# Kernel optimization log

Hardware: AMD Instinct MI355X
Metric: run time of the kernel (lower is better)

Reference implementation:

```python
import jax, jax.numpy as jnp
import numpy as np

B, T_IN, F, NB = 32768, 3, 6, 10
H = 256
BD = H // 2            # baseline_dim
T_OUT = 5
DIN = F + H + BD       # decoder LSTMCell input size
EPS = 1e-5


def _lstm_cell(x, h, c, W_ih, W_hh, b_ih, b_hh):
    # PyTorch gate order: i, f, g, o
    z = x @ W_ih.T + h @ W_hh.T + b_ih + b_hh
    i, f, g, o = jnp.split(z, 4, axis=-1)
    c = jax.nn.sigmoid(f) * c + jax.nn.sigmoid(i) * jnp.tanh(g)
    h = jax.nn.sigmoid(o) * jnp.tanh(c)
    return h, c


def _lstm_layer(xs, W_ih, W_hh, b_ih, b_hh):
    # xs: (T, B, D_in) -> outputs (T, B, H), final (h, c)
    Bn = xs.shape[1]
    h0 = jnp.zeros((Bn, H), xs.dtype)
    c0 = jnp.zeros((Bn, H), xs.dtype)

    def step(carry, x):
        h, c = carry
        h, c = _lstm_cell(x, h, c, W_ih, W_hh, b_ih, b_hh)
        return (h, c), h

    (hT, cT), ys = jax.lax.scan(step, (h0, c0), xs)
    return ys, hT, cT


def setup_inputs() -> dict:
    key = jax.random.key(0)
    ks = jax.random.split(key, 16)
    s = 0.05
    d = {
        "cbc_input": jax.random.normal(ks[0], (B, T_IN, F), jnp.float32),
        "baseline": jax.random.normal(ks[1], (B, NB), jnp.float32),
        # encoder LSTM layer 0 / 1
        "W_ih0": jax.random.normal(ks[2], (4 * H, F), jnp.float32) * s,
        "W_hh0": jax.random.normal(ks[3], (4 * H, H), jnp.float32) * s,
        "b_ih0": jnp.zeros((4 * H,), jnp.float32),
        "b_hh0": jnp.zeros((4 * H,), jnp.float32),
        "W_ih1": jax.random.normal(ks[4], (4 * H, H), jnp.float32) * s,
        "W_hh1": jax.random.normal(ks[5], (4 * H, H), jnp.float32) * s,
        "b_ih1": jnp.zeros((4 * H,), jnp.float32),
        "b_hh1": jnp.zeros((4 * H,), jnp.float32),
        # baseline encoder: Linear + ReLU + LayerNorm
        "Wb": jax.random.normal(ks[6], (BD, NB), jnp.float32) * s,
        "bb": jnp.zeros((BD,), jnp.float32),
        "ln_g": jnp.ones((BD,), jnp.float32),
        "ln_b": jnp.zeros((BD,), jnp.float32),
        # Bahdanau attention
        "W1a": jax.random.normal(ks[7], (H, H), jnp.float32) * s,
        "b1a": jnp.zeros((H,), jnp.float32),
        "W2a": jax.random.normal(ks[8], (H, H), jnp.float32) * s,
        "b2a": jnp.zeros((H,), jnp.float32),
        "va": jax.random.normal(ks[9], (1, H), jnp.float32) * s,
        "ba": jnp.zeros((1,), jnp.float32),
        # decoder LSTMCell
        "Wd_ih": jax.random.normal(ks[10], (4 * H, DIN), jnp.float32) * s,
        "Wd_hh": jax.random.normal(ks[11], (4 * H, H), jnp.float32) * s,
        "bd_ih": jnp.zeros((4 * H,), jnp.float32),
        "bd_hh": jnp.zeros((4 * H,), jnp.float32),
        # output projection MLP
        "Wo1": jax.random.normal(ks[12], (BD, H), jnp.float32) * s,
        "bo1": jnp.zeros((BD,), jnp.float32),
        "Wo2": jax.random.normal(ks[13], (F, BD), jnp.float32) * s,
        "bo2": jnp.zeros((F,), jnp.float32),
    }
    return d


def reference(cbc_input, baseline, W_ih0, W_hh0, b_ih0, b_hh0,
              W_ih1, W_hh1, b_ih1, b_hh1, Wb, bb, ln_g, ln_b,
              W1a, b1a, W2a, b2a, va, ba,
              Wd_ih, Wd_hh, bd_ih, bd_hh, Wo1, bo1, Wo2, bo2):
    # ---- encoder (2-layer LSTM, batch_first; eval mode so no dropout) ----
    xs = jnp.swapaxes(cbc_input, 0, 1)                      # (T, B, F)
    y0, _, _ = _lstm_layer(xs, W_ih0, W_hh0, b_ih0, b_hh0)  # (T, B, H)
    y1, hT, cT = _lstm_layer(y0, W_ih1, W_hh1, b_ih1, b_hh1)
    encoder_outputs = jnp.swapaxes(y1, 0, 1)                # (B, T, H)

    # ---- baseline encoder: Linear -> ReLU -> LayerNorm ----
    z = jax.nn.relu(baseline @ Wb.T + bb)
    mu = jnp.mean(z, axis=-1, keepdims=True)
    var = jnp.mean((z - mu) ** 2, axis=-1, keepdims=True)
    baseline_repr = (z - mu) * jax.lax.rsqrt(var + EPS) * ln_g + ln_b  # (B, BD)

    enc_proj = encoder_outputs @ W2a.T + b2a                # (B, T, H) precomputed
    last_cbc0 = cbc_input[:, -1, :]                         # (B, F)

    def step(carry, _):
        h, c, last_cbc = carry
        # Bahdanau attention
        q = (h @ W1a.T + b1a)[:, None, :]                   # (B, 1, H)
        scores = jnp.tanh(q + enc_proj) @ va.T + ba         # (B, T, 1)
        weights = jax.nn.softmax(scores, axis=1)
        context = jnp.sum(weights * encoder_outputs, axis=1)  # (B, H)
        dec_in = jnp.concatenate([last_cbc, context, baseline_repr], axis=1)
        h, c = _lstm_cell(dec_in, h, c, Wd_ih, Wd_hh, bd_ih, bd_hh)
        delta = jax.nn.relu(h @ Wo1.T + bo1) @ Wo2.T + bo2
        pred = last_cbc + delta
        return (h, c, pred), pred

    _, preds = jax.lax.scan(step, (hT, cT, last_cbc0), None, length=T_OUT)
    return jnp.swapaxes(preds, 0, 1)                        # (B, 5, F)
```

## Files before the change

### kernel.cpp

```cpp
#include <hip/hip_runtime.h>

typedef unsigned short u16;
typedef __bf16 bf16x8 __attribute__((ext_vector_type(8)));
typedef float f32x4 __attribute__((ext_vector_type(4)));

#define BATCH 32768L

__device__ __forceinline__ u16 f2b(float f) {
  union { float f; unsigned int u; } v; v.f = f;
  unsigned int r = v.u + 0x7fffu + ((v.u >> 16) & 1u);
  return (u16)(r >> 16);
}
__device__ __forceinline__ float b2f(u16 h) {
  union { unsigned int u; float f; } v; v.u = ((unsigned int)h) << 16;
  return v.f;
}
__device__ __forceinline__ float sigf(float x) { return 1.f / (1.f + __expf(-x)); }
__device__ __forceinline__ float tanh_f(float x) { return 2.f / (1.f + __expf(-2.f * x)) - 1.f; }

__device__ __forceinline__ void gload16(const void* g, void* l) {
  __builtin_amdgcn_global_load_lds((const __attribute__((address_space(1))) unsigned int*)g,
                                   (__attribute__((address_space(3))) unsigned int*)l,
                                   16, 0, 0);
}

struct PrepP {
  const float* s[9]; u16* d[9]; int sc[9]; int dc[9]; long n[9];
  const float* ba[3]; const float* bb_[3]; float* bo[3];
};

__global__ void prep_kernel(PrepP p, long cvtTotal, long total) {
  for (long i = (long)blockIdx.x * blockDim.x + threadIdx.x; i < total;
       i += (long)gridDim.x * blockDim.x) {
    if (i < cvtTotal) {
      long off = i; int sg = 0;
      while (off >= p.n[sg]) { off -= p.n[sg]; ++sg; }
      long r = off / p.dc[sg]; int c = (int)(off - r * p.dc[sg]);
      p.d[sg][off] = (c < p.sc[sg]) ? f2b(p.s[sg][r * (long)p.sc[sg] + c]) : (u16)0;
    } else {
      long j = i - cvtTotal; int sg = (int)(j >> 10); int k = (int)(j & 1023);
      p.bo[sg][k] = p.ba[sg][k] + p.bb_[sg][k];
    }
  }
}

template <int EPI, int NG>
__global__ __launch_bounds__(256, 2)
void mfma_gemm4(const u16* __restrict__ A1, long lda1, int K1,
                const u16* __restrict__ W1, int wld1,
                const u16* __restrict__ A2, long lda2, int K2,
                const u16* __restrict__ W2, int wld2,
                int gs, int ys, const float* __restrict__ bias,
                u16* __restrict__ out0, int ldo, int relu,
                const float* __restrict__ cprev, float* __restrict__ cout,
                u16* __restrict__ hout, int ldh)
{
  __shared__ u16 As[3][128 * 32];
  __shared__ u16 Bs[3][NG * 64 * 32];
  const int tid = threadIdx.x;
  const int l = tid & 63, w = tid >> 6;
  const long bm = (long)blockIdx.x * 128;
  const int yb = blockIdx.y;

  const int nch1 = K1 >> 5;
  const int nch2 = A2 ? (K2 >> 5) : 0;
  const int nt = nch1 + nch2;

  f32x4 acc[8][NG];
#pragma unroll
  for (int rf = 0; rf < 8; ++rf)
#pragma unroll
    for (int g = 0; g < NG; ++g) acc[rf][g] = (f32x4){0.f, 0.f, 0.f, 0.f};

  const int l4q = l >> 2;
  const int swzs = ((l & 3) ^ ((l >> 2) & 3)) * 16;

  const char* pA[2];
  const char* pB[NG];
  auto initA = [&](const u16* A, long lda) {
#pragma unroll
    for (int c = 0; c < 2; ++c)
      pA[c] = (const char*)A + ((bm + w * 32 + c * 16 + l4q) * lda) * 2 + swzs;
  };
  auto initB = [&](const u16* W, int wld) {
#pragma unroll
    for (int c = 0; c < NG; ++c) {
      const int brow = w * (NG * 16) + c * 16 + l4q;
      const long wrow = (long)(brow >> 6) * gs + (long)yb * ys + (brow & 63);
      pB[c] = (const char*)W + (wrow * (long)wld) * 2 + swzs;
    }
  };
  auto stage = [&](int buf) {
#pragma unroll
    for (int c = 0; c < 2; ++c) {
      gload16(pA[c], &As[buf][(w * 32 + c * 16) * 32]);
      pA[c] += 64;
    }
#pragma unroll
    for (int c = 0; c < NG; ++c) {
      gload16(pB[c], &Bs[buf][(w * (NG * 16) + c * 16) * 32]);
      pB[c] += 64;
    }
  };

  initA(A1, lda1);
  initB(W1, wld1);
  stage(0);
  if (A2 && nch1 == 1) { initA(A2, lda2); initB(W2, wld2); }
  if (nt > 1) stage(1);

  const int rb = l & 15;
  const int koff = ((l >> 4) ^ (l & 3)) * 8;
  int bufR = 0, bufS = 2;
  for (int ch = 0; ch < nt; ++ch) {
    if (ch + 1 < nt) {
      asm volatile("s_waitcnt vmcnt(%0)\n\ts_barrier" :: "i"(2 + NG) : "memory");
    } else {
      asm volatile("s_waitcnt vmcnt(0)\n\ts_barrier" ::: "memory");
    }
    const int s = ch + 2;
    if (s < nt) {
      if (A2 && s == nch1) { initA(A2, lda2); initB(W2, wld2); }
      stage(bufS);
    }
    const u16* Ab = As[bufR];
    const u16* Bb = Bs[bufR];
    bf16x8 af[8];
#pragma unroll
    for (int rf = 0; rf < 8; ++rf)
      af[rf] = *(const bf16x8*)&Ab[(rf * 16 + rb) * 32 + koff];
#pragma unroll
    for (int g = 0; g < NG; ++g) {
      bf16x8 bfr = *(const bf16x8*)&Bb[(g * 64 + w * 16 + rb) * 32 + koff];
#pragma unroll
      for (int rf = 0; rf < 8; ++rf)
        acc[rf][g] = __builtin_amdgcn_mfma_f32_16x16x32_bf16(af[rf], bfr, acc[rf][g], 0, 0, 0);
    }
    bufR = (bufR == 2) ? 0 : bufR + 1;
    bufS = (bufS == 2) ? 0 : bufS + 1;
  }

  const int colb = l & 15;
  const int rq = l >> 4;
  if constexpr (EPI == 0) {
#pragma unroll
    for (int g = 0; g < NG; ++g) {
      const int wrow = g * gs + yb * ys + w * 16 + colb;
      const float bi = bias[wrow];
#pragma unroll
      for (int rf = 0; rf < 8; ++rf) {
#pragma unroll
        for (int r = 0; r < 4; ++r) {
          const long row = bm + rf * 16 + rq * 4 + r;
          float vv = acc[rf][g][r] + bi;
          if (relu) vv = fmaxf(vv, 0.f);
          out0[row * (long)ldo + wrow] = f2b(vv);
        }
      }
    }
  } else {
    const int cb = yb * 64 + w * 16 + colb;
    const float b_i = bias[cb];
    const float b_f = bias[256 + cb];
    const float b_g = bias[512 + cb];
    const float b_o = bias[768 + cb];
#pragma unroll
    for (int rf = 0; rf < 8; ++rf) {
#pragma unroll
      for (int r = 0; r < 4; ++r) {
        const long row = bm + rf * 16 + rq * 4 + r;
        const float zi = acc[rf][0][r] + b_i;
        const float zf = acc[rf][1][r] + b_f;
        const float zg = acc[rf][2][r] + b_g;
        const float zo = acc[rf][3][r] + b_o;
        const float cp = cprev ? cprev[row * 256 + cb] : 0.f;
        const float cn = sigf(zf) * cp + sigf(zi) * tanh_f(zg);
        const float hn = sigf(zo) * tanh_f(cn);
        cout[row * 256 + cb] = cn;
        hout[row * (long)ldh + cb] = f2b(hn);
      }
    }
  }
}

__global__ __launch_bounds__(256)
void front_kernel(const float* __restrict__ cbc, const float* __restrict__ baseline,
                  const float* __restrict__ Wb, const float* __restrict__ bb,
                  const float* __restrict__ ln_g, const float* __restrict__ ln_b,
                  u16* __restrict__ dec_in, u16* __restrict__ xbf)
{
  __shared__ float wbs[1280];
  __shared__ float bbs[128], lgs[128], lbs[128];
  const int tid = threadIdx.x;
  for (int i = tid; i < 1280; i += 256) wbs[i] = Wb[i];
  if (tid < 128) { bbs[tid] = bb[tid]; lgs[tid] = ln_g[tid]; lbs[tid] = ln_b[tid]; }
  __syncthreads();
  const int l = tid & 63, w = tid >> 6;
  const long row = (long)blockIdx.x * 4 + w;
#pragma unroll
  for (int e = l; e < 96; e += 64) {
    const int t = e >> 5, c = e & 31;
    xbf[(row * 3 + t) * 32 + c] = (c < 6) ? f2b(cbc[row * 18 + t * 6 + c]) : (u16)0;
  }
  if (l < 6) dec_in[row * 416 + l] = f2b(cbc[row * 18 + 12 + l]);
  else if (l < 32) dec_in[row * 416 + 390 + (l - 6)] = 0;
  float bl[10];
#pragma unroll
  for (int k = 0; k < 10; ++k) bl[k] = baseline[row * 10 + k];
  const int c0 = l, c1 = l + 64;
  float z0 = bbs[c0], z1 = bbs[c1];
#pragma unroll
  for (int k = 0; k < 10; ++k) { z0 += bl[k] * wbs[c0 * 10 + k]; z1 += bl[k] * wbs[c1 * 10 + k]; }
  z0 = fmaxf(z0, 0.f); z1 = fmaxf(z1, 0.f);
  float s = z0 + z1, sq = z0 * z0 + z1 * z1;
#pragma unroll
  for (int m = 32; m; m >>= 1) { s += __shfl_xor(s, m); sq += __shfl_xor(sq, m); }
  const float mu = s * (1.f / 128.f);
  const float var = sq * (1.f / 128.f) - mu * mu;
  const float rs = rsqrtf(var + 1e-5f);
  dec_in[row * 416 + 262 + c0] = f2b((z0 - mu) * rs * lgs[c0] + lbs[c0]);
  dec_in[row * 416 + 262 + c1] = f2b((z1 - mu) * rs * lgs[c1] + lbs[c1]);
}

__global__ __launch_bounds__(256)
void attn_kernel(const u16* __restrict__ q, const u16* __restrict__ ep,
                 const u16* __restrict__ eo, const float* __restrict__ va,
                 const float* __restrict__ ba, u16* __restrict__ dec_in)
{
  const int tid = threadIdx.x;
  const int l = tid & 63, w = tid >> 6;
  const long row = (long)blockIdx.x * 4 + w;
  const int c = l * 4;
  float qv[4], vav[4];
  {
    ushort4 qu = *(const ushort4*)&q[row * 256 + c];
    qv[0] = b2f(qu.x); qv[1] = b2f(qu.y); qv[2] = b2f(qu.z); qv[3] = b2f(qu.w);
    float4 vv = *(const float4*)&va[c];
    vav[0] = vv.x; vav[1] = vv.y; vav[2] = vv.z; vav[3] = vv.w;
  }
  float s[3];
#pragma unroll
  for (int t = 0; t < 3; ++t) {
    ushort4 eu = *(const ushort4*)&ep[row * 768 + t * 256 + c];
    float p = tanh_f(qv[0] + b2f(eu.x)) * vav[0]
            + tanh_f(qv[1] + b2f(eu.y)) * vav[1]
            + tanh_f(qv[2] + b2f(eu.z)) * vav[2]
            + tanh_f(qv[3] + b2f(eu.w)) * vav[3];
#pragma unroll
    for (int m = 32; m; m >>= 1) p += __shfl_xor(p, m);
    s[t] = p + ba[0];
  }
  const float mx = fmaxf(s[0], fmaxf(s[1], s[2]));
  const float e0 = __expf(s[0] - mx), e1 = __expf(s[1] - mx), e2 = __expf(s[2] - mx);
  const float inv = 1.f / (e0 + e1 + e2);
  const float w0 = e0 * inv, w1 = e1 * inv, w2 = e2 * inv;
  const ushort4 a0 = *(const ushort4*)&eo[row * 768 + 0 * 256 + c];
  const ushort4 a1 = *(const ushort4*)&eo[row * 768 + 1 * 256 + c];
  const ushort4 a2 = *(const ushort4*)&eo[row * 768 + 2 * 256 + c];
  u16* dp = &dec_in[row * 416 + 6 + c];
  dp[0] = f2b(w0 * b2f(a0.x) + w1 * b2f(a1.x) + w2 * b2f(a2.x));
  dp[1] = f2b(w0 * b2f(a0.y) + w1 * b2f(a1.y) + w2 * b2f(a2.y));
  dp[2] = f2b(w0 * b2f(a0.z) + w1 * b2f(a1.z) + w2 * b2f(a2.z));
  dp[3] = f2b(w0 * b2f(a0.w) + w1 * b2f(a1.w) + w2 * b2f(a2.w));
}

__global__ __launch_bounds__(256)
void delta_kernel(const u16* __restrict__ t1, const float* __restrict__ Wo2,
                  const float* __restrict__ bo2, const float* __restrict__ lastp, int lstride,
                  float* __restrict__ outp, int ostride, u16* __restrict__ dec_in)
{
  __shared__ float w2s[768];
  __shared__ float part[64][4][6];
  const int tid = threadIdx.x;
  for (int i = tid; i < 768; i += 256) w2s[i] = Wo2[i];
  __syncthreads();
  const int rw = tid >> 2, q = tid & 3;
  const long row = (long)blockIdx.x * 64 + rw;
  float p[6] = {0.f, 0.f, 0.f, 0.f, 0.f, 0.f};
  const u16* tp = &t1[row * 128 + q * 32];
#pragma unroll
  for (int it = 0; it < 4; ++it) {
    int4 chunk = *(const int4*)&tp[it * 8];
    const u16* cu = (const u16*)&chunk;
#pragma unroll
    for (int e = 0; e < 8; ++e) {
      const float tv = b2f(cu[e]);
      const int k = q * 32 + it * 8 + e;
#pragma unroll
      for (int j = 0; j < 6; ++j) p[j] += tv * w2s[j * 128 + k];
    }
  }
#pragma unroll
  for (int j = 0; j < 6; ++j) part[rw][q][j] = p[j];
  __syncthreads();
  if (tid < 64) {
    const long r2 = (long)blockIdx.x * 64 + tid;
#pragma unroll
    for (int j = 0; j < 6; ++j) {
      const float d = bo2[j] + part[tid][0][j] + part[tid][1][j] + part[tid][2][j] + part[tid][3][j];
      const float pr = lastp[r2 * lstride + j] + d;
      outp[r2 * ostride + j] = pr;
      dec_in[r2 * 416 + j] = f2b(pr);
    }
  }
}

extern "C" void kernel_launch(void* const* d_in, const int* in_sizes, int n_in,
                              void* d_out, int out_size, void* d_ws, size_t ws_size,
                              hipStream_t stream) {
  const float* cbc   = (const float*)d_in[0];
  const float* base  = (const float*)d_in[1];
  const float* W_ih0 = (const float*)d_in[2];
  const float* W_hh0 = (const float*)d_in[3];
  const float* b_ih0 = (const float*)d_in[4];
  const float* b_hh0 = (const float*)d_in[5];
  const float* W_ih1 = (const float*)d_in[6];
  const float* W_hh1 = (const float*)d_in[7];
  const float* b_ih1 = (const float*)d_in[8];
  const float* b_hh1 = (const float*)d_in[9];
  const float* Wb    = (const float*)d_in[10];
  const float* bb    = (const float*)d_in[11];
  const float* ln_g  = (const float*)d_in[12];
  const float* ln_b  = (const float*)d_in[13];
  const float* W1a   = (const float*)d_in[14];
  const float* b1a   = (const float*)d_in[15];
  const float* W2a   = (const float*)d_in[16];
  const float* b2a   = (const float*)d_in[17];
  const float* va    = (const float*)d_in[18];
  const float* ba    = (const float*)d_in[19];
  const float* Wd_ih = (const float*)d_in[20];
  const float* Wd_hh = (const float*)d_in[21];
  const float* bd_ih = (const float*)d_in[22];
  const float* bd_hh = (const float*)d_in[23];
  const float* Wo1   = (const float*)d_in[24];
  const float* bo1   = (const float*)d_in[25];
  const float* Wo2   = (const float*)d_in[26];
  const float* bo2   = (const float*)d_in[27];
  float* out = (float*)d_out;
  (void)in_sizes; (void)n_in; (void)out_size;

  unsigned char* wsb = (unsigned char*)d_ws;
  size_t off = 0;
  auto alloc = [&](size_t bytes) -> void* {
    void* p = wsb + off;
    off += (bytes + 255) & ~(size_t)255;
    return p;
  };
  u16* wih0b = (u16*)alloc(1024 * 32 * 2);
  u16* whh0b = (u16*)alloc(1024 * 256 * 2);
  u16* wih1b = (u16*)alloc(1024 * 256 * 2);
  u16* whh1b = (u16*)alloc(1024 * 256 * 2);
  u16* wdihb = (u16*)alloc(1024 * 416 * 2);
  u16* wdhhb = (u16*)alloc(1024 * 256 * 2);
  u16* w1ab  = (u16*)alloc(256 * 256 * 2);
  u16* w2ab  = (u16*)alloc(256 * 256 * 2);
  u16* wo1b  = (u16*)alloc(128 * 256 * 2);
  float* bsum0 = (float*)alloc(1024 * 4);
  float* bsum1 = (float*)alloc(1024 * 4);
  float* bsumd = (float*)alloc(1024 * 4);

  const long perRow = 6656;
  long avail = (long)ws_size - (long)off - 32768;
  long R = avail > 0 ? avail / perRow : 128;
  R &= ~127L;
  if (R > BATCH) R = BATCH;
  if (R < 128) R = 128;

  u16* xbf    = (u16*)alloc((size_t)R * 96 * 2);
  u16* y0     = (u16*)alloc((size_t)R * 768 * 2);
  u16* y1     = (u16*)alloc((size_t)R * 768 * 2);
  float* cbuf = (float*)alloc((size_t)R * 256 * 4);
  u16* hdec0  = (u16*)alloc((size_t)R * 256 * 2);
  u16* hdec1  = (u16*)alloc((size_t)R * 256 * 2);
  u16* qt1    = (u16*)alloc((size_t)R * 256 * 2);
  u16* dec_in = (u16*)alloc((size_t)R * 416 * 2);

  {
    PrepP p;
    const float* ss[9] = {W_ih0, W_hh0, W_ih1, W_hh1, Wd_ih, Wd_hh, W1a, W2a, Wo1};
    u16* dd[9]         = {wih0b, whh0b, wih1b, whh1b, wdihb, wdhhb, w1ab, w2ab, wo1b};
    int scv[9]         = {6, 256, 256, 256, 390, 256, 256, 256, 256};
    int dcv[9]         = {32, 256, 256, 256, 416, 256, 256, 256, 256};
    long rows[9]       = {1024, 1024, 1024, 1024, 1024, 1024, 256, 256, 128};
    long cvtTotal = 0;
    for (int i = 0; i < 9; ++i) {
      p.s[i] = ss[i]; p.d[i] = dd[i]; p.sc[i] = scv[i]; p.dc[i] = dcv[i];
      p.n[i] = rows[i] * dcv[i]; cvtTotal += p.n[i];
    }
    p.ba[0] = b_ih0; p.bb_[0] = b_hh0; p.bo[0] = bsum0;
    p.ba[1] = b_ih1; p.bb_[1] = b_hh1; p.bo[1] = bsum1;
    p.ba[2] = bd_ih; p.bb_[2] = bd_hh; p.bo[2] = bsumd;
    prep_kernel<<<dim3(2048), dim3(256), 0, stream>>>(p, cvtTotal, cvtTotal + 3072);
  }

  const dim3 blk(256);

  for (long r0 = 0; r0 < BATCH; r0 += R) {
    const long Rc = (BATCH - r0 < R) ? (BATCH - r0) : R;
    const unsigned nb = (unsigned)(Rc / 128);
    const dim3 gcell(nb, 4);
    const float* cbc_c  = cbc + r0 * 18;
    const float* base_c = base + r0 * 10;
    float* out_c = out + r0 * 30;

    front_kernel<<<dim3((unsigned)(Rc / 4)), blk, 0, stream>>>(
        cbc_c, base_c, Wb, bb, ln_g, ln_b, dec_in, xbf);

    for (int t = 0; t < 3; ++t) {
      const u16* a2 = t ? (y0 + (t - 1) * 256) : nullptr;
      mfma_gemm4<1, 4><<<gcell, blk, 0, stream>>>(
          xbf + t * 32, 96, 32, wih0b, 32,
          a2, 768, 256, whh0b, 256,
          256, 64, bsum0,
          nullptr, 0, 0,
          (t ? cbuf : nullptr), cbuf, y0 + t * 256, 768);
    }
    for (int t = 0; t < 3; ++t) {
      const u16* a2 = t ? (y1 + (t - 1) * 256) : nullptr;
      mfma_gemm4<1, 4><<<gcell, blk, 0, stream>>>(
          y0 + t * 256, 768, 256, wih1b, 256,
          a2, 768, 256, whh1b, 256,
          256, 64, bsum1,
          nullptr, 0, 0,
          (t ? cbuf : nullptr), cbuf, y1 + t * 256, 768);
    }
    mfma_gemm4<0, 4><<<dim3(nb * 3, 1), blk, 0, stream>>>(
        y1, 256, 256, w2ab, 256,
        nullptr, 0, 0, nullptr, 0,
        64, 0, b2a,
        y0, 256, 0,
        nullptr, nullptr, nullptr, 0);

    const u16* hcur = y1 + 2 * 256; long hld = 768;
    for (int s = 0; s < 5; ++s) {
      mfma_gemm4<0, 2><<<dim3(nb, 2), blk, 0, stream>>>(
          hcur, hld, 256, w1ab, 256,
          nullptr, 0, 0, nullptr, 0,
          64, 128, b1a,
          qt1, 256, 0,
          nullptr, nullptr, nullptr, 0);
      attn_kernel<<<dim3((unsigned)(Rc / 4)), blk, 0, stream>>>(qt1, y0, y1, va, ba, dec_in);
      u16* hnext = (s & 1) ? hdec1 : hdec0;
      mfma_gemm4<1, 4><<<gcell, blk, 0, stream>>>(
          dec_in, 416, 416, wdihb, 416,
          hcur, hld, 256, wdhhb, 256,
          256, 64, bsumd,
          nullptr, 0, 0,
          cbuf, cbuf, hnext, 256);
      hcur = hnext; hld = 256;
      mfma_gemm4<0, 2><<<dim3(nb, 1), blk, 0, stream>>>(
          hcur, 256, 256, wo1b, 256,
          nullptr, 0, 0, nullptr, 0,
          64, 0, bo1,
          qt1, 128, 1,
          nullptr, nullptr, nullptr, 0);
      const float* lastp = (s == 0) ? (cbc_c + 12) : (out_c + (long)(s - 1) * 6);
      const int lstr = (s == 0) ? 18 : 30;
      delta_kernel<<<dim3((unsigned)(Rc / 64)), blk, 0, stream>>>(
          qt1, Wo2, bo2, lastp, lstr, out_c + (long)s * 6, 30, dec_in);
    }
  }
}
```

Measured before the change: 1.038 ms.

## Halve GEMM row tile, use double buffering, fold bias into accumulators, fast intrinsics

```diff
diff --git a/kernel.cpp b/kernel.cpp
--- a/kernel.cpp
+++ b/kernel.cpp
@@ -15,8 +15,13 @@
   union { unsigned int u; float f; } v; v.u = ((unsigned int)h) << 16;
   return v.f;
 }
-__device__ __forceinline__ float sigf(float x) { return 1.f / (1.f + __expf(-x)); }
-__device__ __forceinline__ float tanh_f(float x) { return 2.f / (1.f + __expf(-2.f * x)) - 1.f; }
+__device__ __forceinline__ float rcpf(float x) { return __builtin_amdgcn_rcpf(x); }
+__device__ __forceinline__ float sigf(float x) {
+  return rcpf(1.f + __builtin_amdgcn_exp2f(-1.442695041f * x));
+}
+__device__ __forceinline__ float tanh_f(float x) {
+  return 1.f - 2.f * rcpf(1.f + __builtin_amdgcn_exp2f(2.885390082f * x));
+}
 
 __device__ __forceinline__ void gload16(const void* g, void* l) {
   __builtin_amdgcn_global_load_lds((const __attribute__((address_space(1))) unsigned int*)g,
@@ -45,8 +50,8 @@
 }
 
 template <int EPI, int NG>
-__global__ __launch_bounds__(256, 2)
-void mfma_gemm4(const u16* __restrict__ A1, long lda1, int K1,
+__global__ __launch_bounds__(256, 3)
+void mfma_gemm6(const u16* __restrict__ A1, long lda1, int K1,
                 const u16* __restrict__ W1, int wld1,
                 const u16* __restrict__ A2, long lda2, int K2,
                 const u16* __restrict__ W2, int wld2,
@@ -55,50 +60,52 @@
                 const float* __restrict__ cprev, float* __restrict__ cout,
                 u16* __restrict__ hout, int ldh)
 {
-  __shared__ u16 As[3][128 * 32];
-  __shared__ u16 Bs[3][NG * 64 * 32];
+  __shared__ u16 As[2][64 * 32];
+  __shared__ u16 Bs[2][NG * 64 * 32];
   const int tid = threadIdx.x;
   const int l = tid & 63, w = tid >> 6;
-  const long bm = (long)blockIdx.x * 128;
+  const long bm = (long)blockIdx.x * 64;
   const int yb = blockIdx.y;
 
   const int nch1 = K1 >> 5;
   const int nch2 = A2 ? (K2 >> 5) : 0;
   const int nt = nch1 + nch2;
 
-  f32x4 acc[8][NG];
-#pragma unroll
-  for (int rf = 0; rf < 8; ++rf)
-#pragma unroll
-    for (int g = 0; g < NG; ++g) acc[rf][g] = (f32x4){0.f, 0.f, 0.f, 0.f};
+  const int colb = l & 15, rq = l >> 4;
+
+  f32x4 acc[4][NG];
+  {
+    float bw[NG];
+#pragma unroll
+    for (int g = 0; g < NG; ++g) bw[g] = bias[g * gs + yb * ys + w * 16 + colb];
+#pragma unroll
+    for (int rf = 0; rf < 4; ++rf)
+#pragma unroll
+      for (int g = 0; g < NG; ++g) acc[rf][g] = (f32x4){bw[g], bw[g], bw[g], bw[g]};
+  }
 
   const int l4q = l >> 2;
   const int swzs = ((l & 3) ^ ((l >> 2) & 3)) * 16;
 
-  const char* pA[2];
+  const char* pA;
   const char* pB[NG];
   auto initA = [&](const u16* A, long lda) {
-#pragma unroll
-    for (int c = 0; c < 2; ++c)
-      pA[c] = (const char*)A + ((bm + w * 32 + c * 16 + l4q) * lda) * 2 + swzs;
+    pA = (const char*)A + ((bm + w * 16 + l4q) * lda) * 2 + swzs;
   };
   auto initB = [&](const u16* W, int wld) {
 #pragma unroll
     for (int c = 0; c < NG; ++c) {
-      const int brow = w * (NG * 16) + c * 16 + l4q;
+      const int brow = (w * NG + c) * 16 + l4q;
       const long wrow = (long)(brow >> 6) * gs + (long)yb * ys + (brow & 63);
       pB[c] = (const char*)W + (wrow * (long)wld) * 2 + swzs;
     }
   };
   auto stage = [&](int buf) {
-#pragma unroll
-    for (int c = 0; c < 2; ++c) {
-      gload16(pA[c], &As[buf][(w * 32 + c * 16) * 32]);
-      pA[c] += 64;
-    }
+    gload16(pA, &As[buf][(w * 16) * 32]);
+    pA += 64;
 #pragma unroll
     for (int c = 0; c < NG; ++c) {
-      gload16(pB[c], &Bs[buf][(w * (NG * 16) + c * 16) * 32]);
+      gload16(pB[c], &Bs[buf][((w * NG + c) * 16) * 32]);
       pB[c] += 64;
     }
   };
@@ -106,73 +113,57 @@
   initA(A1, lda1);
   initB(W1, wld1);
   stage(0);
-  if (A2 && nch1 == 1) { initA(A2, lda2); initB(W2, wld2); }
-  if (nt > 1) stage(1);
 
   const int rb = l & 15;
   const int koff = ((l >> 4) ^ (l & 3)) * 8;
-  int bufR = 0, bufS = 2;
+  int cur = 0;
   for (int ch = 0; ch < nt; ++ch) {
+    __syncthreads();
     if (ch + 1 < nt) {
-      asm volatile("s_waitcnt vmcnt(%0)\n\ts_barrier" :: "i"(2 + NG) : "memory");
-    } else {
-      asm volatile("s_waitcnt vmcnt(0)\n\ts_barrier" ::: "memory");
-    }
-    const int s = ch + 2;
-    if (s < nt) {
-      if (A2 && s == nch1) { initA(A2, lda2); initB(W2, wld2); }
-      stage(bufS);
-    }
-    const u16* Ab = As[bufR];
-    const u16* Bb = Bs[bufR];
-    bf16x8 af[8];
-#pragma unroll
-    for (int rf = 0; rf < 8; ++rf)
+      if (A2 && ch + 1 == nch1) { initA(A2, lda2); initB(W2, wld2); }
+      stage(cur ^ 1);
+    }
+    const u16* Ab = As[cur];
+    const u16* Bb = Bs[cur];
+    bf16x8 af[4];
+#pragma unroll
+    for (int rf = 0; rf < 4; ++rf)
       af[rf] = *(const bf16x8*)&Ab[(rf * 16 + rb) * 32 + koff];
 #pragma unroll
     for (int g = 0; g < NG; ++g) {
       bf16x8 bfr = *(const bf16x8*)&Bb[(g * 64 + w * 16 + rb) * 32 + koff];
 #pragma unroll
-      for (int rf = 0; rf < 8; ++rf)
+      for (int rf = 0; rf < 4; ++rf)
         acc[rf][g] = __builtin_amdgcn_mfma_f32_16x16x32_bf16(af[rf], bfr, acc[rf][g], 0, 0, 0);
     }
-    bufR = (bufR == 2) ? 0 : bufR + 1;
-    bufS = (bufS == 2) ? 0 : bufS + 1;
-  }
-
-  const int colb = l & 15;
-  const int rq = l >> 4;
+    cur ^= 1;
+  }
+
   if constexpr (EPI == 0) {
 #pragma unroll
     for (int g = 0; g < NG; ++g) {
       const int wrow = g * gs + yb * ys + w * 16 + colb;
-      const float bi = bias[wrow];
-#pragma unroll
-      for (int rf = 0; rf < 8; ++rf) {
+#pragma unroll
+      for (int rf = 0; rf < 4; ++rf) {
 #pragma unroll
         for (int r = 0; r < 4; ++r) {
-          const long row = bm + rf * 16 + rq * 4 + r;
-          float vv = acc[rf][g][r] + bi;
+          float vv = acc[rf][g][r];
           if (relu) vv = fmaxf(vv, 0.f);
-          out0[row * (long)ldo + wrow] = f2b(vv);
+          out0[(bm + rf * 16 + rq * 4 + r) * (long)ldo + wrow] = f2b(vv);
         }
       }
     }
   } else {
-    const int cb = yb * 64 + w * 16 + colb;
-    const float b_i = bias[cb];
-    const float b_f = bias[256 + cb];
-    const float b_g = bias[512 + cb];
-    const float b_o = bias[768 + cb];
-#pragma unroll
-    for (int rf = 0; rf < 8; ++rf) {
+    const int cb = yb * ys + w * 16 + colb;
+#pragma unroll
+    for (int rf = 0; rf < 4; ++rf) {
 #pragma unroll
       for (int r = 0; r < 4; ++r) {
         const long row = bm + rf * 16 + rq * 4 + r;
-        const float zi = acc[rf][0][r] + b_i;
-        const float zf = acc[rf][1][r] + b_f;
-        const float zg = acc[rf][2][r] + b_g;
-        const float zo = acc[rf][3][r] + b_o;
+        const float zi = acc[rf][0][r];
+        const float zf = acc[rf][1][r];
+        const float zg = acc[rf][2][r];
+        const float zo = acc[rf][3][r];
         const float cp = cprev ? cprev[row * 256 + cb] : 0.f;
         const float cn = sigf(zf) * cp + sigf(zi) * tanh_f(zg);
         const float hn = sigf(zo) * tanh_f(cn);
@@ -252,7 +243,7 @@
   }
   const float mx = fmaxf(s[0], fmaxf(s[1], s[2]));
   const float e0 = __expf(s[0] - mx), e1 = __expf(s[1] - mx), e2 = __expf(s[2] - mx);
-  const float inv = 1.f / (e0 + e1 + e2);
+  const float inv = rcpf(e0 + e1 + e2);
   const float w0 = e0 * inv, w1 = e1 * inv, w2 = e2 * inv;
   const ushort4 a0 = *(const ushort4*)&eo[row * 768 + 0 * 256 + c];
   const ushort4 a1 = *(const ushort4*)&eo[row * 768 + 1 * 256 + c];
@@ -361,10 +352,10 @@
 
   const long perRow = 6656;
   long avail = (long)ws_size - (long)off - 32768;
-  long R = avail > 0 ? avail / perRow : 128;
-  R &= ~127L;
+  long R = avail > 0 ? avail / perRow : 256;
+  R &= ~255L;
   if (R > BATCH) R = BATCH;
-  if (R < 128) R = 128;
+  if (R < 256) R = 256;
 
   u16* xbf    = (u16*)alloc((size_t)R * 96 * 2);
   u16* y0     = (u16*)alloc((size_t)R * 768 * 2);
@@ -397,7 +388,7 @@
 
   for (long r0 = 0; r0 < BATCH; r0 += R) {
     const long Rc = (BATCH - r0 < R) ? (BATCH - r0) : R;
-    const unsigned nb = (unsigned)(Rc / 128);
+    const unsigned nb = (unsigned)(Rc / 64);
     const dim3 gcell(nb, 4);
     const float* cbc_c  = cbc + r0 * 18;
     const float* base_c = base + r0 * 10;
@@ -408,7 +399,7 @@
 
     for (int t = 0; t < 3; ++t) {
       const u16* a2 = t ? (y0 + (t - 1) * 256) : nullptr;
-      mfma_gemm4<1, 4><<<gcell, blk, 0, stream>>>(
+      mfma_gemm6<1, 4><<<gcell, blk, 0, stream>>>(
           xbf + t * 32, 96, 32, wih0b, 32,
           a2, 768, 256, whh0b, 256,
           256, 64, bsum0,
@@ -417,14 +408,14 @@
     }
     for (int t = 0; t < 3; ++t) {
       const u16* a2 = t ? (y1 + (t - 1) * 256) : nullptr;
-      mfma_gemm4<1, 4><<<gcell, blk, 0, stream>>>(
+      mfma_gemm6<1, 4><<<gcell, blk, 0, stream>>>(
           y0 + t * 256, 768, 256, wih1b, 256,
           a2, 768, 256, whh1b, 256,
           256, 64, bsum1,
           nullptr, 0, 0,
           (t ? cbuf : nullptr), cbuf, y1 + t * 256, 768);
     }
-    mfma_gemm4<0, 4><<<dim3(nb * 3, 1), blk, 0, stream>>>(
+    mfma_gemm6<0, 4><<<dim3(nb * 3, 1), blk, 0, stream>>>(
         y1, 256, 256, w2ab, 256,
         nullptr, 0, 0, nullptr, 0,
         64, 0, b2a,
@@ -433,22 +424,22 @@
 
     const u16* hcur = y1 + 2 * 256; long hld = 768;
     for (int s = 0; s < 5; ++s) {
-      mfma_gemm4<0, 2><<<dim3(nb, 2), blk, 0, stream>>>(
+      mfma_gemm6<0, 4><<<dim3(nb, 1), blk, 0, stream>>>(
           hcur, hld, 256, w1ab, 256,
           nullptr, 0, 0, nullptr, 0,
-          64, 128, b1a,
+          64, 0, b1a,
           qt1, 256, 0,
           nullptr, nullptr, nullptr, 0);
       attn_kernel<<<dim3((unsigned)(Rc / 4)), blk, 0, stream>>>(qt1, y0, y1, va, ba, dec_in);
       u16* hnext = (s & 1) ? hdec1 : hdec0;
-      mfma_gemm4<1, 4><<<gcell, blk, 0, stream>>>(
+      mfma_gemm6<1, 4><<<gcell, blk, 0, stream>>>(
           dec_in, 416, 416, wdihb, 416,
           hcur, hld, 256, wdhhb, 256,
           256, 64, bsumd,
           nullptr, 0, 0,
           cbuf, cbuf, hnext, 256);
       hcur = hnext; hld = 256;
-      mfma_gemm4<0, 2><<<dim3(nb, 1), blk, 0, stream>>>(
+      mfma_gemm6<0, 2><<<dim3(nb, 1), blk, 0, stream>>>(
           hcur, 256, 256, wo1b, 256,
           nullptr, 0, 0, nullptr, 0,
           64, 0, bo1,
```

Result: faster. 964.6 us (-7.1%).
